# Optimization experiments

Hardware: AMD Instinct MI355X
Metric: run time of the kernel (lower is better)

Reference implementation:

```python
import jax, jax.numpy as jnp
import numpy as np

N_NODES = 50000
N_EDGES = 500000
N_GRAPHS = 1024
NF = 128          # node_feature
DIST_DIM = 64
SH_DIM = 64
SH_IN = 9         # spherical_harmonics_l**2, l=3
IN_DIM = 92
N_LAYERS = 5
RBF_BINS = 64
RBF_VMIN, RBF_VMAX = 0.125, 1.4


def _lin(x, W, b):
    return x @ W + b


def setup_inputs() -> dict:
    key = jax.random.key(0)
    ks = jax.random.split(key, 32)
    s = lambda fan_in: 1.0 / np.sqrt(fan_in)

    def W(k, i, o):
        return jax.random.uniform(k, (i, o), jnp.float32, -s(i), s(i))

    inp = {
        "x": jax.random.normal(ks[0], (N_NODES, IN_DIM), jnp.float32),
        "edge_index": jax.random.randint(ks[1], (2, N_EDGES), 0, N_NODES, jnp.int64),
        "sh": jax.random.normal(ks[2], (N_EDGES, SH_IN), jnp.float32),
        "edge_dist": jax.random.uniform(ks[3], (N_EDGES,), jnp.float32, 0.2, 1.0),
        "batch": jnp.sort(jax.random.randint(ks[4], (N_NODES,), 0, N_GRAPHS, jnp.int64)),
        # atom embedding
        "W_emb": W(ks[5], IN_DIM, NF), "b_emb": jnp.zeros((NF,), jnp.float32),
        # sh_mlp: 9 -> 32 -> 64
        "sh_W1": W(ks[6], SH_IN, 32), "sh_b1": jnp.zeros((32,), jnp.float32),
        "sh_W2": W(ks[7], 32, SH_DIM), "sh_b2": jnp.zeros((SH_DIM,), jnp.float32),
        # rbf tail: 64 -> 64 -> 64
        "rbf_W1": W(ks[8], RBF_BINS, 64), "rbf_b1": jnp.zeros((64,), jnp.float32),
        "rbf_W2": W(ks[9], 64, DIST_DIM), "rbf_b2": jnp.zeros((DIST_DIM,), jnp.float32),
        # SFTConv (CGConv-style gated message) stacked over layers: z dim = 3*NF
        "Wg": jnp.stack([W(jax.random.fold_in(ks[10], l), 3 * NF, NF) for l in range(N_LAYERS)]),
        "bg": jnp.zeros((N_LAYERS, NF), jnp.float32),
        "Wc": jnp.stack([W(jax.random.fold_in(ks[11], l), 3 * NF, NF) for l in range(N_LAYERS)]),
        "bc": jnp.zeros((N_LAYERS, NF), jnp.float32),
        # readout fc: 128 -> 128 -> 1
        "fc_W1": W(ks[12], NF, 128), "fc_b1": jnp.zeros((128,), jnp.float32),
        "fc_W2": W(ks[13], 128, 1), "fc_b2": jnp.zeros((1,), jnp.float32),
    }
    return inp


def reference(x, edge_index, sh, edge_dist, batch,
              W_emb, b_emb, sh_W1, sh_b1, sh_W2, sh_b2,
              rbf_W1, rbf_b1, rbf_W2, rbf_b2,
              Wg, bg, Wc, bc, fc_W1, fc_b1, fc_W2, fc_b2):
    # atom embedding: [N, 92] -> [N, 128]
    h = _lin(x, W_emb, b_emb)

    # spherical harmonics edge MLP: [E, 9] -> [E, 64]
    sh_e = _lin(jax.nn.silu(_lin(sh, sh_W1, sh_b1)), sh_W2, sh_b2)

    # RBF expansion of inverse distance (no_grad in torch -> stop_gradient)
    inv_d = jax.lax.stop_gradient(1.0 / edge_dist)[:, None]       # [E, 1]
    centers = jnp.linspace(RBF_VMIN, RBF_VMAX, RBF_BINS, dtype=jnp.float32)
    gamma = 1.0 / (centers[1] - centers[0]) ** 2
    rbf = jnp.exp(-gamma * (inv_d - centers) ** 2)                # [E, 64]
    dist_e = _lin(jax.nn.silu(_lin(rbf, rbf_W1, rbf_b1)), rbf_W2, rbf_b2)

    edge_attr = jnp.concatenate([dist_e, sh_e], axis=-1)          # [E, 128]

    src, dst = edge_index[0], edge_index[1]
    n_nodes = h.shape[0]
    for l in range(Wg.shape[0]):
        # gated CGConv-style message: z = [h_dst, h_src, e]  -> [E, 384]
        z = jnp.concatenate([h[dst], h[src], edge_attr], axis=-1)
        m = jax.nn.sigmoid(z @ Wg[l] + bg[l]) * jax.nn.softplus(z @ Wc[l] + bc[l])
        agg = jax.ops.segment_sum(m, dst, num_segments=n_nodes)   # [N, 128]
        h = h + agg

    # scatter-mean readout over batch ids
    sums = jax.ops.segment_sum(h, batch, num_segments=N_GRAPHS)   # [G, 128]
    counts = jax.ops.segment_sum(jnp.ones((n_nodes,), h.dtype), batch, num_segments=N_GRAPHS)
    pooled = sums / jnp.maximum(counts, 1.0)[:, None]

    out = _lin(jax.nn.silu(_lin(pooled, fc_W1, fc_b1)), fc_W2, fc_b2)  # [G, 1]
    return out.squeeze(-1)
```

## Files before the change

kernel.cpp:

```cpp
#include <hip/hip_runtime.h>

typedef __bf16 bf16x8 __attribute__((ext_vector_type(8)));
typedef __bf16 bf16x4 __attribute__((ext_vector_type(4)));
typedef float  f32x4  __attribute__((ext_vector_type(4)));
typedef float  f32x2  __attribute__((ext_vector_type(2)));

#define N_NODES  50000
#define N_EDGES  500000
#define EB       128
#define EP       500096
#define NCH      12
#define N_GRAPHS 1024
#define NF       128
#define IN_DIM   92
#define N_LAYERS 5
#define SPANMAX  256

__device__ __forceinline__ float sigmoidf_(float x) { return 1.0f / (1.0f + __expf(-x)); }
__device__ __forceinline__ float softplusf_(float x) {
    return fmaxf(x, 0.0f) + __logf(1.0f + __expf(-fabsf(x)));
}
__device__ __forceinline__ float siluf_(float x) { return x * sigmoidf_(x); }

__global__ void __launch_bounds__(256) k_fold(const float* __restrict__ Wg,
    const float* __restrict__ Wc, const float* __restrict__ rbW2,
    const float* __restrict__ rbB2, const float* __restrict__ shW2,
    const float* __restrict__ shB2, const float* __restrict__ bg,
    const float* __restrict__ bc, float* __restrict__ Wfold,
    float* __restrict__ bF) {
    int lg = blockIdx.x, l = lg >> 1, g = lg & 1;
    const float* W = (g ? Wc : Wg) + (size_t)l * 384 * 128;
    const float* bsrc = (g ? bc : bg) + l * 128;
    int tid = threadIdx.x;
    for (int idx = tid; idx < 96 * 128; idx += 256) {
        int r = idx >> 7, n = idx & 127;
        float s = 0.f;
        if (r < 64) {
            for (int o = 0; o < 64; ++o) s += rbW2[r * 64 + o] * W[(256 + o) * 128 + n];
        } else {
            int j = r - 64;
            for (int o = 0; o < 64; ++o) s += shW2[j * 64 + o] * W[(320 + o) * 128 + n];
        }
        Wfold[(size_t)lg * 12288 + idx] = s;
    }
    if (tid < 128) {
        float s = bsrc[tid];
        for (int o = 0; o < 64; ++o) s += rbB2[o] * W[(256 + o) * 128 + tid];
        for (int o = 0; o < 64; ++o) s += shB2[o] * W[(320 + o) * 128 + tid];
        bF[lg * 128 + tid] = s;
    }
}

__global__ void __launch_bounds__(256) k_prep_w(const float* __restrict__ Wg,
                                                const float* __restrict__ Wc,
                                                const float* __restrict__ Wfold,
                                                __bf16* __restrict__ WeT,
                                                __bf16* __restrict__ WnT) {
    int t = blockIdx.x * 256 + threadIdx.x;
    if (t >= (240 + 640) * 64) return;
    int frag = t >> 6, lane = t & 63;
    int sub = lane >> 4, mm = lane & 15;
    bf16x8 v;
    if (frag < 240) {
        int lg = frag / 24; int r = frag % 24;
        int m = r / 3; int ks = r % 3;
        #pragma unroll
        for (int j = 0; j < 8; ++j) {
            int k = ks * 32 + sub * 8 + j;
            v[j] = (__bf16)Wfold[(size_t)lg * 12288 + (size_t)k * 128 + m * 16 + mm];
        }
        *(bf16x8*)(WeT + (size_t)frag * 512 + lane * 8) = v;
    } else {
        int f2 = frag - 240;
        int l = f2 / 128; int r = f2 % 128;
        int m = r >> 2; int ks = r & 3;
        int F = m * 16 + mm;
        #pragma unroll
        for (int j = 0; j < 8; ++j) {
            int k = ks * 32 + sub * 8 + j;
            float val;
            if      (F < 128) val = Wg[(size_t)l*384*128 + (size_t)k*128 + F];
            else if (F < 256) val = Wc[(size_t)l*384*128 + (size_t)k*128 + (F-128)];
            else if (F < 384) val = Wg[(size_t)l*384*128 + (size_t)(128+k)*128 + (F-256)];
            else              val = Wc[(size_t)l*384*128 + (size_t)(128+k)*128 + (F-384)];
            v[j] = (__bf16)val;
        }
        *(bf16x8*)(WnT + (size_t)f2 * 512 + lane * 8) = v;
    }
}

__global__ void __launch_bounds__(256) k_deg(const int* __restrict__ dstI,
                                             int* __restrict__ deg) {
    int e = blockIdx.x * 256 + threadIdx.x;
    if (e < N_EDGES) atomicAdd(&deg[dstI[e]], 1);
}

__global__ void __launch_bounds__(1024) k_scan(const int* __restrict__ deg,
                                               int* __restrict__ cursor) {
    __shared__ int ps[1024];
    int t = threadIdx.x;
    const int C = (N_NODES + 1023) / 1024;
    int base = t * C;
    int s = 0;
    for (int i = 0; i < C; ++i) { int idx = base + i; if (idx < N_NODES) s += deg[idx]; }
    ps[t] = s;
    __syncthreads();
    for (int off = 1; off < 1024; off <<= 1) {
        int v = 0;
        if (t >= off) v = ps[t - off];
        __syncthreads();
        if (t >= off) ps[t] += v;
        __syncthreads();
    }
    int run = (t > 0) ? ps[t - 1] : 0;
    for (int i = 0; i < C; ++i) {
        int idx = base + i;
        if (idx < N_NODES) { cursor[idx] = run; run += deg[idx]; }
    }
}

__global__ void __launch_bounds__(256) k_scatter(const int* __restrict__ srcI,
                                                 const int* __restrict__ dstI,
                                                 int* __restrict__ cursor,
                                                 int* __restrict__ perm,
                                                 int* __restrict__ dstS,
                                                 int* __restrict__ srcS) {
    int e = blockIdx.x * 256 + threadIdx.x;
    if (e >= N_EDGES) return;
    int d = dstI[e];
    int p = atomicAdd(&cursor[d], 1);
    perm[p] = e;
    dstS[p] = d;
    srcS[p] = srcI[e];
}

__global__ void __launch_bounds__(128) k_pad(int* __restrict__ dstS,
                                             int* __restrict__ srcS,
                                             char* __restrict__ ea2) {
    int i = threadIdx.x;
    if (i < EP - N_EDGES) {
        dstS[N_EDGES + i] = N_NODES;
        srcS[N_EDGES + i] = 0;
        uint4 z = {0, 0, 0, 0};
        for (int p = 0; p < NCH; ++p)
            *(uint4*)(ea2 + ((size_t)p * EP + N_EDGES + i) * 16) = z;
    }
}

__global__ void __launch_bounds__(256) k_embed(const float* __restrict__ x,
                                               const float* __restrict__ W,
                                               const float* __restrict__ b,
                                               float* __restrict__ h) {
    int tid = threadIdx.x;
    int f = tid & 127;
    int nb = blockIdx.x * 8 + (tid >> 7) * 4;
    const float* x0 = x + (size_t)nb * IN_DIM;
    float a0 = b[f], a1 = a0, a2 = a0, a3 = a0;
    #pragma unroll 4
    for (int k = 0; k < IN_DIM; ++k) {
        float wv = W[k * NF + f];
        a0 = fmaf(x0[k], wv, a0);
        a1 = fmaf(x0[IN_DIM + k], wv, a1);
        a2 = fmaf(x0[2 * IN_DIM + k], wv, a2);
        a3 = fmaf(x0[3 * IN_DIM + k], wv, a3);
    }
    float accs[4] = {a0, a1, a2, a3};
    #pragma unroll
    for (int r = 0; r < 4; ++r)
        h[(size_t)(nb + r) * NF + f] = accs[r];
}

__global__ void __launch_bounds__(256) k_edge(const float* __restrict__ sh,
    const float* __restrict__ dist, const int* __restrict__ perm,
    const float* __restrict__ shW1, const float* __restrict__ shB1,
    const float* __restrict__ rbW1, const float* __restrict__ rbB1,
    char* __restrict__ ea2) {
    __shared__ float wf[4480];
    int tid = threadIdx.x;
    int p = blockIdx.x * 256 + tid;
    bool pv = p < N_EDGES;
    int e = pv ? perm[p] : 0;
    float dv = dist[e];
    float shv[9];
    #pragma unroll
    for (int i = 0; i < 9; ++i) shv[i] = sh[(size_t)e * 9 + i];
    for (int i = tid; i < 288;  i += 256) wf[i]        = shW1[i];
    for (int i = tid; i < 32;   i += 256) wf[288 + i]  = shB1[i];
    for (int i = tid; i < 4096; i += 256) wf[320 + i]  = rbW1[i];
    for (int i = tid; i < 64;   i += 256) wf[4416 + i] = rbB1[i];
    __syncthreads();
    if (!pv) return;

    const float* W1 = wf + 320; const float* B1 = wf + 4416;
    float invd = 1.0f / dv;
    const float step = (1.4f - 0.125f) / 63.0f;
    const float gam = 1.0f / (step * step);
    float hid[64];
    #pragma unroll
    for (int j = 0; j < 64; ++j) hid[j] = B1[j];
    for (int i = 0; i < 64; ++i) {
        float c = 0.125f + i * step;
        float d = invd - c;
        float r = __expf(-gam * d * d);
        #pragma unroll
        for (int j = 0; j < 64; ++j) hid[j] += r * W1[i * 64 + j];
    }
    #pragma unroll
    for (int o8 = 0; o8 < 8; ++o8) {
        bf16x8 v;
        #pragma unroll
        for (int j = 0; j < 8; ++j) v[j] = (__bf16)siluf_(hid[o8 * 8 + j]);
        *(bf16x8*)(ea2 + ((size_t)o8 * EP + p) * 16) = v;
    }
    const float* sW1 = wf; const float* sB1 = wf + 288;
    float h2[32];
    #pragma unroll
    for (int j = 0; j < 32; ++j) h2[j] = sB1[j];
    #pragma unroll
    for (int i = 0; i < 9; ++i) {
        float si = shv[i];
        #pragma unroll
        for (int j = 0; j < 32; ++j) h2[j] += si * sW1[i * 32 + j];
    }
    #pragma unroll
    for (int o8 = 0; o8 < 4; ++o8) {
        bf16x8 v;
        #pragma unroll
        for (int j = 0; j < 8; ++j) v[j] = (__bf16)siluf_(h2[o8 * 8 + j]);
        *(bf16x8*)(ea2 + ((size_t)(8 + o8) * EP + p) * 16) = v;
    }
}

template <typename TD>
__global__ void __launch_bounds__(256) k_node(const float* __restrict__ h,
                                              const __bf16* __restrict__ WnT,
                                              const float* __restrict__ bgl,
                                              const float* __restrict__ bcl,
                                              TD* __restrict__ NBd,
                                              __bf16* __restrict__ NBs, int layer) {
    int tid = threadIdx.x, lane = tid & 63, w = tid >> 6;
    int sub = lane >> 4, rA = lane & 15;
    int node0 = blockIdx.x * 32;
    bf16x8 Bf[2][4];
    #pragma unroll
    for (int nt = 0; nt < 2; ++nt)
        #pragma unroll
        for (int ks = 0; ks < 4; ++ks) {
            int node = min(node0 + nt * 16 + rA, N_NODES - 1);
            const float* hr = h + (size_t)node * 128 + ks * 32 + sub * 8;
            f32x4 u0 = *(const f32x4*)hr;
            f32x4 u1 = *(const f32x4*)(hr + 4);
            bf16x8 bv;
            bv[0] = (__bf16)u0[0]; bv[1] = (__bf16)u0[1];
            bv[2] = (__bf16)u0[2]; bv[3] = (__bf16)u0[3];
            bv[4] = (__bf16)u1[0]; bv[5] = (__bf16)u1[1];
            bv[6] = (__bf16)u1[2]; bv[7] = (__bf16)u1[3];
            Bf[nt][ks] = bv;
        }
    const __bf16* Wbase = WnT + (size_t)layer * 128 * 512;
    f32x4 acc[8][2];
    f32x4 zz = {0.f, 0.f, 0.f, 0.f};
    #pragma unroll
    for (int mt = 0; mt < 8; ++mt) { acc[mt][0] = zz; acc[mt][1] = zz; }
    for (int mt = 0; mt < 8; ++mt) {
        int gm = w * 8 + mt;
        bf16x8 Af[4];
        #pragma unroll
        for (int ks = 0; ks < 4; ++ks)
            Af[ks] = *(const bf16x8*)(Wbase + (size_t)(gm * 4 + ks) * 512 + lane * 8);
        #pragma unroll
        for (int nt = 0; nt < 2; ++nt) {
            f32x4 a = acc[mt][nt];
            #pragma unroll
            for (int ks = 0; ks < 4; ++ks)
                a = __builtin_amdgcn_mfma_f32_16x16x32_bf16(Af[ks], Bf[nt][ks], a, 0, 0, 0);
            acc[mt][nt] = a;
        }
    }
    #pragma unroll
    for (int mt = 0; mt < 8; ++mt) {
        int F = (w * 8 + mt) * 16 + sub * 4;
        f32x4 bias = zz;
        if (w == 0)      bias = *(const f32x4*)(bgl + F);
        else if (w == 1) bias = *(const f32x4*)(bcl + (F - 128));
        #pragma unroll
        for (int nt = 0; nt < 2; ++nt) {
            int node = node0 + nt * 16 + rA;
            if (node >= N_NODES) continue;
            f32x4 vv = acc[mt][nt];
            vv[0] += bias[0]; vv[1] += bias[1]; vv[2] += bias[2]; vv[3] += bias[3];
            if (w < 2) {
                if constexpr (sizeof(TD) == 4) {
                    *(f32x4*)(NBd + (size_t)node * 256 + F) = vv;
                } else {
                    bf16x4 bv;
                    bv[0] = (__bf16)vv[0]; bv[1] = (__bf16)vv[1];
                    bv[2] = (__bf16)vv[2]; bv[3] = (__bf16)vv[3];
                    *(bf16x4*)((__bf16*)NBd + (size_t)node * 256 + F) = bv;
                }
            } else {
                bf16x4 bv;
                bv[0] = (__bf16)vv[0]; bv[1] = (__bf16)vv[1];
                bv[2] = (__bf16)vv[2]; bv[3] = (__bf16)vv[3];
                *(bf16x4*)(NBs + (size_t)node * 256 + (F - 256)) = bv;
            }
        }
    }
}

template <typename TD>
__device__ __forceinline__ f32x4 ld_nb4(const TD* p) {
    if constexpr (sizeof(TD) == 4) {
        return *(const f32x4*)p;
    } else {
        bf16x4 t = *(const bf16x4*)p;
        f32x4 r;
        r[0] = (float)t[0]; r[1] = (float)t[1]; r[2] = (float)t[2]; r[3] = (float)t[3];
        return r;
    }
}

template <typename TD>
__global__ void __launch_bounds__(512, 4) k_msg(
    const char* __restrict__ ea2, const int* __restrict__ dstS,
    const int* __restrict__ srcS, const __bf16* __restrict__ WeT,
    const TD* __restrict__ NBd, const __bf16* __restrict__ NBs,
    float* __restrict__ h, int layer)
{
    __shared__ __align__(16) float mF[EB * 128];
    __shared__ int rs[SPANMAX], re[SPANMAX];
    int tid = threadIdx.x, lane = tid & 63, w = tid >> 6;
    int sub = lane >> 4, rA = lane & 15;
    int e0 = blockIdx.x * EB;
    int F = w * 16 + sub * 4;
    int n0 = dstS[e0];

    if (tid < EB) {
        int d = dstS[e0 + tid];
        int di = min(d - n0, SPANMAX - 1);
        if (tid == 0 || dstS[e0 + tid - 1] != d) {
            rs[di] = tid;
            if (tid > 0) {
                int dp = dstS[e0 + tid - 1];
                for (int g = dp + 1; g < d && (g - n0) < SPANMAX; ++g) {
                    rs[g - n0] = 0; re[g - n0] = 0;
                }
            }
        }
        if (tid == EB - 1 || dstS[e0 + tid + 1] != d) re[di] = tid + 1;
    }

    bf16x8 Ag[3], Ac[3];
    {
        const __bf16* bg_ = WeT + (size_t)(((layer * 2 + 0) * 8 + w) * 3) * 512;
        const __bf16* bc_ = WeT + (size_t)(((layer * 2 + 1) * 8 + w) * 3) * 512;
        #pragma unroll
        for (int ks = 0; ks < 3; ++ks) {
            Ag[ks] = *(const bf16x8*)(bg_ + ks * 512 + lane * 8);
            Ac[ks] = *(const bf16x8*)(bc_ + ks * 512 + lane * 8);
        }
    }

    const char* eb0 = ea2 + ((size_t)(0 + sub) * EP + e0 + rA) * 16;
    const char* eb1 = ea2 + ((size_t)(4 + sub) * EP + e0 + rA) * 16;
    const char* eb2 = ea2 + ((size_t)(8 + sub) * EP + e0 + rA) * 16;
    const int* srcp = srcS + e0 + rA;
    const int* dstp = dstS + e0 + rA;
    char* mfp = (char*)mF + rA * 512 + ((w * 64 + sub * 16) ^ ((rA & 7) << 4));

    f32x4 zz = {0.f, 0.f, 0.f, 0.f};
    bf16x8 bfr[2][3];
    bf16x4 gs[2], cs[2];
    f32x4  gd[2], cd[2];

    {
        int src = srcp[0], dstc = min(dstp[0], N_NODES - 1);
        bfr[0][0] = *(const bf16x8*)(eb0);
        bfr[0][1] = *(const bf16x8*)(eb1);
        bfr[0][2] = *(const bf16x8*)(eb2);
        gs[0] = *(const bf16x4*)(NBs + (size_t)src * 256 + F);
        cs[0] = *(const bf16x4*)(NBs + (size_t)src * 256 + 128 + F);
        gd[0] = ld_nb4(NBd + (size_t)dstc * 256 + F);
        cd[0] = ld_nb4(NBd + (size_t)dstc * 256 + 128 + F);
    }
    #pragma unroll
    for (int nt = 0; nt < EB / 16; ++nt) {
        int cur = nt & 1, nxt = cur ^ 1;
        if (nt + 1 < EB / 16) {
            int src = srcp[(nt + 1) * 16], dstc = min(dstp[(nt + 1) * 16], N_NODES - 1);
            bfr[nxt][0] = *(const bf16x8*)(eb0 + (nt + 1) * 256);
            bfr[nxt][1] = *(const bf16x8*)(eb1 + (nt + 1) * 256);
            bfr[nxt][2] = *(const bf16x8*)(eb2 + (nt + 1) * 256);
            gs[nxt] = *(const bf16x4*)(NBs + (size_t)src * 256 + F);
            cs[nxt] = *(const bf16x4*)(NBs + (size_t)src * 256 + 128 + F);
            gd[nxt] = ld_nb4(NBd + (size_t)dstc * 256 + F);
            cd[nxt] = ld_nb4(NBd + (size_t)dstc * 256 + 128 + F);
        }
        f32x4 aG = zz, aC = zz;
        #pragma unroll
        for (int ks = 0; ks < 3; ++ks) {
            aG = __builtin_amdgcn_mfma_f32_16x16x32_bf16(Ag[ks], bfr[cur][ks], aG, 0, 0, 0);
            aC = __builtin_amdgcn_mfma_f32_16x16x32_bf16(Ac[ks], bfr[cur][ks], aC, 0, 0, 0);
        }
        f32x4 mv;
        #pragma unroll
        for (int r = 0; r < 4; ++r) {
            float gi = aG[r] + gd[cur][r] + (float)gs[cur][r];
            float ci = aC[r] + cd[cur][r] + (float)cs[cur][r];
            mv[r] = sigmoidf_(gi) * softplusf_(ci);
        }
        *(f32x4*)(mfp + nt * 8192) = mv;
    }
    __syncthreads();
    int span = min(dstS[e0 + EB - 1] - n0 + 1, SPANMAX);
    int items = span * 32;
    for (int it = tid; it < items; it += 512) {
        int ln = it >> 5, fq = it & 31;
        int rs_ = rs[ln], re_ = re[ln];
        f32x4 s = zz;
        for (int e = rs_; e < re_; ++e) {
            f32x4 v = *(const f32x4*)((char*)mF + e * 512 + ((fq * 16) ^ ((e & 7) << 4)));
            s[0] += v[0]; s[1] += v[1]; s[2] += v[2]; s[3] += v[3];
        }
        int node = n0 + ln;
        float* dp = h + (size_t)node * 128 + fq * 4;
        if (ln == 0 || ln == span - 1) {
            atomicAdd(dp + 0, s[0]); atomicAdd(dp + 1, s[1]);
            atomicAdd(dp + 2, s[2]); atomicAdd(dp + 3, s[3]);
        } else {
            dp[0] += s[0]; dp[1] += s[1]; dp[2] += s[2]; dp[3] += s[3];
        }
    }
}

__global__ void __launch_bounds__(128) k_readout(const float* __restrict__ h,
    const int* __restrict__ batch, const float* __restrict__ W1,
    const float* __restrict__ b1, const float* __restrict__ W2,
    const float* __restrict__ b2, float* __restrict__ out) {
    int g = blockIdx.x, tid = threadIdx.x;
    __shared__ int se[2];
    __shared__ float pl[NF];
    __shared__ float red[2];
    if (tid < 2) {
        int target = g + tid;
        int lo = 0, hi = N_NODES;
        while (lo < hi) { int mid = (lo + hi) >> 1; if (batch[mid] < target) lo = mid + 1; else hi = mid; }
        se[tid] = lo;
    }
    __syncthreads();
    int s = se[0], e = se[1];
    float sum = 0.0f;
    for (int n = s; n < e; ++n) sum += h[(size_t)n * NF + tid];
    float cnt = (float)max(e - s, 1);
    pl[tid] = sum / cnt;
    __syncthreads();
    float acc = b1[tid];
    for (int c = 0; c < NF; ++c) acc += pl[c] * W1[c * NF + tid];
    float hid = siluf_(acc);
    float v = hid * W2[tid];
    #pragma unroll
    for (int off = 32; off > 0; off >>= 1) v += __shfl_down(v, off);
    if ((tid & 63) == 0) red[tid >> 6] = v;
    __syncthreads();
    if (tid == 0) out[g] = red[0] + red[1] + b2[0];
}

extern "C" void kernel_launch(void* const* d_in, const int* in_sizes, int n_in,
                              void* d_out, int out_size, void* d_ws, size_t ws_size,
                              hipStream_t stream) {
    const float* x     = (const float*)d_in[0];
    const int*   eidx  = (const int*)d_in[1];
    const float* sh    = (const float*)d_in[2];
    const float* edist = (const float*)d_in[3];
    const int*   batch = (const int*)d_in[4];
    const float* W_emb = (const float*)d_in[5];
    const float* b_emb = (const float*)d_in[6];
    const float* shW1  = (const float*)d_in[7];
    const float* shB1  = (const float*)d_in[8];
    const float* shW2  = (const float*)d_in[9];
    const float* shB2  = (const float*)d_in[10];
    const float* rbW1  = (const float*)d_in[11];
    const float* rbB1  = (const float*)d_in[12];
    const float* rbW2  = (const float*)d_in[13];
    const float* rbB2  = (const float*)d_in[14];
    const float* Wg    = (const float*)d_in[15];
    const float* bg    = (const float*)d_in[16];
    const float* Wc    = (const float*)d_in[17];
    const float* bc    = (const float*)d_in[18];
    const float* fcW1  = (const float*)d_in[19];
    const float* fcb1  = (const float*)d_in[20];
    const float* fcW2  = (const float*)d_in[21];
    const float* fcb2  = (const float*)d_in[22];
    const int* srcI = eidx;
    const int* dstI = eidx + N_EDGES;

    char* ws = (char*)d_ws;
    float*  h     = (float*)(ws + 0);
    char*   ea2   = (char*)(ws + 25600512);
    int*    dstS  = (int*)(ws + 121618944);
    int*    srcS  = (int*)(ws + 123619328);
    int*    deg   = (int*)(ws + 125619712);
    int*    curs  = (int*)(ws + 125819712);
    int*    perm  = (int*)(ws + 126019712);
    __bf16* WeT   = (__bf16*)(ws + 128019712);
    __bf16* WnT   = (__bf16*)(ws + 128265472);
    float*  Wfold = (float*)(ws + 128920832);
    float*  bF    = (float*)(ws + 129412352);
    __bf16* NBs   = (__bf16*)(ws + 129417472);
    void*   NBd   = (void*)(ws + 155017472);
    bool nbf32 = (ws_size >= 206217472ULL);

    hipMemsetAsync(deg, 0, (size_t)N_NODES * sizeof(int), stream);
    k_fold<<<10, 256, 0, stream>>>(Wg, Wc, rbW2, rbB2, shW2, shB2, bg, bc, Wfold, bF);
    k_prep_w<<<220, 256, 0, stream>>>(Wg, Wc, Wfold, WeT, WnT);
    k_embed<<<N_NODES / 8, 256, 0, stream>>>(x, W_emb, b_emb, h);
    k_deg<<<(N_EDGES + 255) / 256, 256, 0, stream>>>(dstI, deg);
    k_scan<<<1, 1024, 0, stream>>>(deg, curs);
    k_scatter<<<(N_EDGES + 255) / 256, 256, 0, stream>>>(srcI, dstI, curs, perm, dstS, srcS);
    k_edge<<<(N_EDGES + 255) / 256, 256, 0, stream>>>(sh, edist, perm, shW1, shB1,
                                                      rbW1, rbB1, ea2);
    k_pad<<<1, 128, 0, stream>>>(dstS, srcS, ea2);
    for (int l = 0; l < N_LAYERS; ++l) {
        const float* bgF = bF + (l * 2 + 0) * 128;
        const float* bcF = bF + (l * 2 + 1) * 128;
        if (nbf32) {
            k_node<float><<<(N_NODES + 31) / 32, 256, 0, stream>>>(
                h, WnT, bgF, bcF, (float*)NBd, NBs, l);
            k_msg<float><<<EP / EB, 512, 0, stream>>>(
                ea2, dstS, srcS, WeT, (const float*)NBd, NBs, h, l);
        } else {
            k_node<__bf16><<<(N_NODES + 31) / 32, 256, 0, stream>>>(
                h, WnT, bgF, bcF, (__bf16*)NBd, NBs, l);
            k_msg<__bf16><<<EP / EB, 512, 0, stream>>>(
                ea2, dstS, srcS, WeT, (const __bf16*)NBd, NBs, h, l);
        }
    }
    k_readout<<<N_GRAPHS, 128, 0, stream>>>(h, batch, fcW1, fcb1, fcW2, fcb2, (float*)d_out);
}
```

Before: 1.211 ms.

## Interleave node projections into one bf16 buffer and pack src/dst index pairs

The per-node projections for the dst gate/core and src gate/core parts are written into one interleaved bf16 row of 512 values. Each message lane can then fetch its dst and src contributions with two 16-byte loads instead of four scattered ones. Src and dst indices are packed into an int2 array so each edge needs one index load. The fp32 dst-path option is removed, so dst terms are always bf16, which costs some precision. The __launch_bounds__ occupancy hint on k_msg is also dropped.

Measured after the change: 1.187 ms. About the same (-1.9%).

```diff
diff --git a/kernel.cpp b/kernel.cpp
--- a/kernel.cpp
+++ b/kernel.cpp
@@ -3,7 +3,6 @@
 typedef __bf16 bf16x8 __attribute__((ext_vector_type(8)));
 typedef __bf16 bf16x4 __attribute__((ext_vector_type(4)));
 typedef float  f32x4  __attribute__((ext_vector_type(4)));
-typedef float  f32x2  __attribute__((ext_vector_type(2)));
 
 #define N_NODES  50000
 #define N_EDGES  500000
@@ -124,23 +123,23 @@
                                                  int* __restrict__ cursor,
                                                  int* __restrict__ perm,
                                                  int* __restrict__ dstS,
-                                                 int* __restrict__ srcS) {
+                                                 int2* __restrict__ sdS) {
     int e = blockIdx.x * 256 + threadIdx.x;
     if (e >= N_EDGES) return;
     int d = dstI[e];
     int p = atomicAdd(&cursor[d], 1);
     perm[p] = e;
     dstS[p] = d;
-    srcS[p] = srcI[e];
+    sdS[p] = make_int2(d, srcI[e]);
 }
 
 __global__ void __launch_bounds__(128) k_pad(int* __restrict__ dstS,
-                                             int* __restrict__ srcS,
+                                             int2* __restrict__ sdS,
                                              char* __restrict__ ea2) {
     int i = threadIdx.x;
     if (i < EP - N_EDGES) {
         dstS[N_EDGES + i] = N_NODES;
-        srcS[N_EDGES + i] = 0;
+        sdS[N_EDGES + i] = make_int2(N_NODES, 0);
         uint4 z = {0, 0, 0, 0};
         for (int p = 0; p < NCH; ++p)
             *(uint4*)(ea2 + ((size_t)p * EP + N_EDGES + i) * 16) = z;
@@ -231,13 +230,11 @@
     }
 }
 
-template <typename TD>
 __global__ void __launch_bounds__(256) k_node(const float* __restrict__ h,
                                               const __bf16* __restrict__ WnT,
                                               const float* __restrict__ bgl,
                                               const float* __restrict__ bcl,
-                                              TD* __restrict__ NBd,
-                                              __bf16* __restrict__ NBs, int layer) {
+                                              __bf16* __restrict__ NB2, int layer) {
     int tid = threadIdx.x, lane = tid & 63, w = tid >> 6;
     int sub = lane >> 4, rA = lane & 15;
     int node0 = blockIdx.x * 32;
@@ -280,59 +277,36 @@
     #pragma unroll
     for (int mt = 0; mt < 8; ++mt) {
         int F = (w * 8 + mt) * 16 + sub * 4;
+        int part = F >> 7;
+        int fq = (F & 127) >> 2;
         f32x4 bias = zz;
-        if (w == 0)      bias = *(const f32x4*)(bgl + F);
-        else if (w == 1) bias = *(const f32x4*)(bcl + (F - 128));
+        if (part == 0)      bias = *(const f32x4*)(bgl + (F & 127));
+        else if (part == 1) bias = *(const f32x4*)(bcl + (F & 127));
         #pragma unroll
         for (int nt = 0; nt < 2; ++nt) {
             int node = node0 + nt * 16 + rA;
             if (node >= N_NODES) continue;
             f32x4 vv = acc[mt][nt];
             vv[0] += bias[0]; vv[1] += bias[1]; vv[2] += bias[2]; vv[3] += bias[3];
-            if (w < 2) {
-                if constexpr (sizeof(TD) == 4) {
-                    *(f32x4*)(NBd + (size_t)node * 256 + F) = vv;
-                } else {
-                    bf16x4 bv;
-                    bv[0] = (__bf16)vv[0]; bv[1] = (__bf16)vv[1];
-                    bv[2] = (__bf16)vv[2]; bv[3] = (__bf16)vv[3];
-                    *(bf16x4*)((__bf16*)NBd + (size_t)node * 256 + F) = bv;
-                }
-            } else {
-                bf16x4 bv;
-                bv[0] = (__bf16)vv[0]; bv[1] = (__bf16)vv[1];
-                bv[2] = (__bf16)vv[2]; bv[3] = (__bf16)vv[3];
-                *(bf16x4*)(NBs + (size_t)node * 256 + (F - 256)) = bv;
-            }
-        }
-    }
-}
-
-template <typename TD>
-__device__ __forceinline__ f32x4 ld_nb4(const TD* p) {
-    if constexpr (sizeof(TD) == 4) {
-        return *(const f32x4*)p;
-    } else {
-        bf16x4 t = *(const bf16x4*)p;
-        f32x4 r;
-        r[0] = (float)t[0]; r[1] = (float)t[1]; r[2] = (float)t[2]; r[3] = (float)t[3];
-        return r;
-    }
-}
-
-template <typename TD>
-__global__ void __launch_bounds__(512, 4) k_msg(
+            bf16x4 bv;
+            bv[0] = (__bf16)vv[0]; bv[1] = (__bf16)vv[1];
+            bv[2] = (__bf16)vv[2]; bv[3] = (__bf16)vv[3];
+            *(bf16x4*)(NB2 + (size_t)node * 512 + fq * 16 + part * 4) = bv;
+        }
+    }
+}
+
+__global__ void __launch_bounds__(512) k_msg(
     const char* __restrict__ ea2, const int* __restrict__ dstS,
-    const int* __restrict__ srcS, const __bf16* __restrict__ WeT,
-    const TD* __restrict__ NBd, const __bf16* __restrict__ NBs,
-    float* __restrict__ h, int layer)
+    const int2* __restrict__ sdS, const __bf16* __restrict__ WeT,
+    const __bf16* __restrict__ NB2, float* __restrict__ h, int layer)
 {
     __shared__ __align__(16) float mF[EB * 128];
     __shared__ int rs[SPANMAX], re[SPANMAX];
     int tid = threadIdx.x, lane = tid & 63, w = tid >> 6;
     int sub = lane >> 4, rA = lane & 15;
     int e0 = blockIdx.x * EB;
-    int F = w * 16 + sub * 4;
+    int fq = w * 4 + sub;
     int n0 = dstS[e0];
 
     if (tid < EB) {
@@ -364,37 +338,33 @@
     const char* eb0 = ea2 + ((size_t)(0 + sub) * EP + e0 + rA) * 16;
     const char* eb1 = ea2 + ((size_t)(4 + sub) * EP + e0 + rA) * 16;
     const char* eb2 = ea2 + ((size_t)(8 + sub) * EP + e0 + rA) * 16;
-    const int* srcp = srcS + e0 + rA;
-    const int* dstp = dstS + e0 + rA;
+    const int2* sdp = sdS + e0 + rA;
     char* mfp = (char*)mF + rA * 512 + ((w * 64 + sub * 16) ^ ((rA & 7) << 4));
 
     f32x4 zz = {0.f, 0.f, 0.f, 0.f};
     bf16x8 bfr[2][3];
-    bf16x4 gs[2], cs[2];
-    f32x4  gd[2], cd[2];
+    bf16x8 dv[2], sv[2];
 
     {
-        int src = srcp[0], dstc = min(dstp[0], N_NODES - 1);
+        int2 sd = sdp[0];
+        int dstc = min(sd.x, N_NODES - 1);
         bfr[0][0] = *(const bf16x8*)(eb0);
         bfr[0][1] = *(const bf16x8*)(eb1);
         bfr[0][2] = *(const bf16x8*)(eb2);
-        gs[0] = *(const bf16x4*)(NBs + (size_t)src * 256 + F);
-        cs[0] = *(const bf16x4*)(NBs + (size_t)src * 256 + 128 + F);
-        gd[0] = ld_nb4(NBd + (size_t)dstc * 256 + F);
-        cd[0] = ld_nb4(NBd + (size_t)dstc * 256 + 128 + F);
+        dv[0] = *(const bf16x8*)(NB2 + (size_t)dstc * 512 + fq * 16);
+        sv[0] = *(const bf16x8*)(NB2 + (size_t)sd.y * 512 + fq * 16 + 8);
     }
     #pragma unroll
     for (int nt = 0; nt < EB / 16; ++nt) {
         int cur = nt & 1, nxt = cur ^ 1;
         if (nt + 1 < EB / 16) {
-            int src = srcp[(nt + 1) * 16], dstc = min(dstp[(nt + 1) * 16], N_NODES - 1);
+            int2 sd = sdp[(nt + 1) * 16];
+            int dstc = min(sd.x, N_NODES - 1);
             bfr[nxt][0] = *(const bf16x8*)(eb0 + (nt + 1) * 256);
             bfr[nxt][1] = *(const bf16x8*)(eb1 + (nt + 1) * 256);
             bfr[nxt][2] = *(const bf16x8*)(eb2 + (nt + 1) * 256);
-            gs[nxt] = *(const bf16x4*)(NBs + (size_t)src * 256 + F);
-            cs[nxt] = *(const bf16x4*)(NBs + (size_t)src * 256 + 128 + F);
-            gd[nxt] = ld_nb4(NBd + (size_t)dstc * 256 + F);
-            cd[nxt] = ld_nb4(NBd + (size_t)dstc * 256 + 128 + F);
+            dv[nxt] = *(const bf16x8*)(NB2 + (size_t)dstc * 512 + fq * 16);
+            sv[nxt] = *(const bf16x8*)(NB2 + (size_t)sd.y * 512 + fq * 16 + 8);
         }
         f32x4 aG = zz, aC = zz;
         #pragma unroll
@@ -405,8 +375,8 @@
         f32x4 mv;
         #pragma unroll
         for (int r = 0; r < 4; ++r) {
-            float gi = aG[r] + gd[cur][r] + (float)gs[cur][r];
-            float ci = aC[r] + cd[cur][r] + (float)cs[cur][r];
+            float gi = aG[r] + (float)dv[cur][r] + (float)sv[cur][r];
+            float ci = aC[r] + (float)dv[cur][4 + r] + (float)sv[cur][4 + r];
             mv[r] = sigmoidf_(gi) * softplusf_(ci);
         }
         *(f32x4*)(mfp + nt * 8192) = mv;
@@ -415,15 +385,15 @@
     int span = min(dstS[e0 + EB - 1] - n0 + 1, SPANMAX);
     int items = span * 32;
     for (int it = tid; it < items; it += 512) {
-        int ln = it >> 5, fq = it & 31;
+        int ln = it >> 5, fqq = it & 31;
         int rs_ = rs[ln], re_ = re[ln];
         f32x4 s = zz;
         for (int e = rs_; e < re_; ++e) {
-            f32x4 v = *(const f32x4*)((char*)mF + e * 512 + ((fq * 16) ^ ((e & 7) << 4)));
+            f32x4 v = *(const f32x4*)((char*)mF + e * 512 + ((fqq * 16) ^ ((e & 7) << 4)));
             s[0] += v[0]; s[1] += v[1]; s[2] += v[2]; s[3] += v[3];
         }
         int node = n0 + ln;
-        float* dp = h + (size_t)node * 128 + fq * 4;
+        float* dp = h + (size_t)node * 128 + fqq * 4;
         if (ln == 0 || ln == span - 1) {
             atomicAdd(dp + 0, s[0]); atomicAdd(dp + 1, s[1]);
             atomicAdd(dp + 2, s[2]); atomicAdd(dp + 3, s[3]);
@@ -498,17 +468,15 @@
     float*  h     = (float*)(ws + 0);
     char*   ea2   = (char*)(ws + 25600512);
     int*    dstS  = (int*)(ws + 121618944);
-    int*    srcS  = (int*)(ws + 123619328);
-    int*    deg   = (int*)(ws + 125619712);
-    int*    curs  = (int*)(ws + 125819712);
-    int*    perm  = (int*)(ws + 126019712);
-    __bf16* WeT   = (__bf16*)(ws + 128019712);
-    __bf16* WnT   = (__bf16*)(ws + 128265472);
-    float*  Wfold = (float*)(ws + 128920832);
-    float*  bF    = (float*)(ws + 129412352);
-    __bf16* NBs   = (__bf16*)(ws + 129417472);
-    void*   NBd   = (void*)(ws + 155017472);
-    bool nbf32 = (ws_size >= 206217472ULL);
+    int2*   sdS   = (int2*)(ws + 123619328);
+    int*    deg   = (int*)(ws + 127620096);
+    int*    curs  = (int*)(ws + 127820096);
+    int*    perm  = (int*)(ws + 128020096);
+    __bf16* WeT   = (__bf16*)(ws + 130020096);
+    __bf16* WnT   = (__bf16*)(ws + 130265856);
+    float*  Wfold = (float*)(ws + 130921216);
+    float*  bF    = (float*)(ws + 131412736);
+    __bf16* NB2   = (__bf16*)(ws + 131417856);
 
     hipMemsetAsync(deg, 0, (size_t)N_NODES * sizeof(int), stream);
     k_fold<<<10, 256, 0, stream>>>(Wg, Wc, rbW2, rbB2, shW2, shB2, bg, bc, Wfold, bF);
@@ -516,24 +484,15 @@
     k_embed<<<N_NODES / 8, 256, 0, stream>>>(x, W_emb, b_emb, h);
     k_deg<<<(N_EDGES + 255) / 256, 256, 0, stream>>>(dstI, deg);
     k_scan<<<1, 1024, 0, stream>>>(deg, curs);
-    k_scatter<<<(N_EDGES + 255) / 256, 256, 0, stream>>>(srcI, dstI, curs, perm, dstS, srcS);
+    k_scatter<<<(N_EDGES + 255) / 256, 256, 0, stream>>>(srcI, dstI, curs, perm, dstS, sdS);
     k_edge<<<(N_EDGES + 255) / 256, 256, 0, stream>>>(sh, edist, perm, shW1, shB1,
                                                       rbW1, rbB1, ea2);
-    k_pad<<<1, 128, 0, stream>>>(dstS, srcS, ea2);
+    k_pad<<<1, 128, 0, stream>>>(dstS, sdS, ea2);
     for (int l = 0; l < N_LAYERS; ++l) {
         const float* bgF = bF + (l * 2 + 0) * 128;
         const float* bcF = bF + (l * 2 + 1) * 128;
-        if (nbf32) {
-            k_node<float><<<(N_NODES + 31) / 32, 256, 0, stream>>>(
-                h, WnT, bgF, bcF, (float*)NBd, NBs, l);
-            k_msg<float><<<EP / EB, 512, 0, stream>>>(
-                ea2, dstS, srcS, WeT, (const float*)NBd, NBs, h, l);
-        } else {
-            k_node<__bf16><<<(N_NODES + 31) / 32, 256, 0, stream>>>(
-                h, WnT, bgF, bcF, (__bf16*)NBd, NBs, l);
-            k_msg<__bf16><<<EP / EB, 512, 0, stream>>>(
-                ea2, dstS, srcS, WeT, (const __bf16*)NBd, NBs, h, l);
-        }
+        k_node<<<(N_NODES + 31) / 32, 256, 0, stream>>>(h, WnT, bgF, bcF, NB2, l);
+        k_msg<<<EP / EB, 512, 0, stream>>>(ea2, dstS, sdS, WeT, NB2, h, l);
     }
     k_readout<<<N_GRAPHS, 128, 0, stream>>>(h, batch, fcW1, fcb1, fcW2, fcb2, (float*)d_out);
 }
```
